# Optimization experiments

Measured on AMD Instinct MI355X. Metric: run time of the kernel, lower is better.

The kernel has to match this reference:

```python
import jax, jax.numpy as jnp
import numpy as np

N, D = 8192, 1024
Q = 4096
DK = 512
DV = 256


def setup_inputs() -> dict:
    key = jax.random.key(0)
    k1, k2, k3, k4, k5, k6 = jax.random.split(key, 6)
    return {
        "search_x": jax.random.normal(k1, (N, D), dtype=jnp.float32),
        "search_y": jax.random.normal(k2, (N, DV), dtype=jnp.float32),
        "query_x": jax.random.normal(k3, (Q, D), dtype=jnp.float32),
        "mask": jax.random.randint(k4, (Q, N), 0, 2, dtype=jnp.int64),
        "Wk": jax.random.normal(k5, (D, DK), dtype=jnp.float32) / np.sqrt(D),
        "Wq": jax.random.normal(k6, (D, DK), dtype=jnp.float32) / np.sqrt(D),
    }


def reference(search_x, search_y, query_x, mask, Wk, Wq):
    # key/query modules: bias-free linear projections (n_keys == 1 after _ensure_key_shape)
    keys = search_x @ Wk            # [N, DK]
    qk = query_x @ Wq               # [Q, DK]
    scale = 1.0 / jnp.sqrt(jnp.asarray(DK, dtype=keys.dtype))
    logits = (qk @ keys.T) * scale  # [Q, N]  (== broadcast mul+sum in original)
    # masked softmax over the search dimension (dim=1)
    m = mask > 0                    # [Q, N]
    neg = jnp.finfo(logits.dtype).min
    p = jax.nn.softmax(jnp.where(m, logits, neg), axis=1)
    p = jnp.where(m, p, 0.0)
    # values = noop_value_module(search_x, search_y) = search_y  [N, DV]
    res = p @ search_y              # [Q, DV]
    return res[:, None, :]          # [Q, n_keys=1, DV], matching original output shape
```

## Files before the change

### kernel.cpp

```cpp
#include <hip/hip_runtime.h>
#include <hip/hip_fp16.h>

typedef _Float16 half4v __attribute__((ext_vector_type(4)));
typedef _Float16 half8v __attribute__((ext_vector_type(8)));
typedef float floatx4 __attribute__((ext_vector_type(4)));

__global__ __launch_bounds__(256) void k_f32_to_f16(const float* __restrict__ in,
                                                    _Float16* __restrict__ out, int n) {
    int i = (blockIdx.x * 256 + threadIdx.x) * 4;
    if (i >= n) return;
    float4 v = *(const float4*)(in + i);
    half4v h;
    h[0] = (_Float16)v.x; h[1] = (_Float16)v.y; h[2] = (_Float16)v.z; h[3] = (_Float16)v.w;
    *(half4v*)(out + i) = h;
}

__global__ __launch_bounds__(256) void k_transpose_f16(const float* __restrict__ in,
                                                       _Float16* __restrict__ out,
                                                       int R, int C) {
    __shared__ float tile[32][33];
    int bc = blockIdx.x * 32;
    int br = blockIdx.y * 32;
    int tx = threadIdx.x & 31, ty = threadIdx.x >> 5;
#pragma unroll
    for (int i = 0; i < 32; i += 8)
        tile[ty + i][tx] = in[(size_t)(br + ty + i) * C + bc + tx];
    __syncthreads();
#pragma unroll
    for (int i = 0; i < 32; i += 8)
        out[(size_t)(bc + ty + i) * R + br + tx] = (_Float16)tile[tx][ty + i];
}

template <bool OUT_F16>
__global__ __launch_bounds__(256) void k_gemm_nt(const _Float16* __restrict__ A,
                                                 const _Float16* __restrict__ B,
                                                 void* __restrict__ C,
                                                 int M, int N, int K, int kChunk,
                                                 float scale) {
    __shared__ _Float16 As[128 * 72];
    __shared__ _Float16 Bs[128 * 72];
    const int tid  = threadIdx.x;
    const int lane = tid & 63;
    const int wave = tid >> 6;
    const int wm   = (wave >> 1) * 64;
    const int wn   = (wave & 1) * 64;
    const int quad = lane >> 4;
    const int lr   = lane & 15;
    const long m0 = (long)blockIdx.y * 128;
    const long n0 = (long)blockIdx.x * 128;
    const int kBegin = blockIdx.z * kChunk;
    const int kEnd   = kBegin + kChunk;

    floatx4 acc[4][4] = {};

    const int sr = tid >> 3;
    const int sc = (tid & 7) * 8;

    for (int kt = kBegin; kt < kEnd; kt += 64) {
        const _Float16* Ap = A + (m0 + sr) * (long)K + kt + sc;
        const _Float16* Bp = B + (n0 + sr) * (long)K + kt + sc;
        uint4 av[4], bv[4];
#pragma unroll
        for (int r = 0; r < 4; ++r) {
            av[r] = *(const uint4*)(Ap + (long)(r * 32) * K);
            bv[r] = *(const uint4*)(Bp + (long)(r * 32) * K);
        }
#pragma unroll
        for (int r = 0; r < 4; ++r) {
            *(uint4*)&As[(sr + r * 32) * 72 + sc] = av[r];
            *(uint4*)&Bs[(sr + r * 32) * 72 + sc] = bv[r];
        }
        __syncthreads();

#pragma unroll
        for (int kk = 0; kk < 64; kk += 32) {
            half8v af[4], bf[4];
#pragma unroll
            for (int i = 0; i < 4; ++i)
                af[i] = *(const half8v*)&As[(wm + i * 16 + lr) * 72 + kk + quad * 8];
#pragma unroll
            for (int j = 0; j < 4; ++j)
                bf[j] = *(const half8v*)&Bs[(wn + j * 16 + lr) * 72 + kk + quad * 8];
#pragma unroll
            for (int i = 0; i < 4; ++i)
#pragma unroll
                for (int j = 0; j < 4; ++j)
                    acc[i][j] = __builtin_amdgcn_mfma_f32_16x16x32_f16(af[i], bf[j], acc[i][j], 0, 0, 0);
        }
        __syncthreads();
    }

#pragma unroll
    for (int i = 0; i < 4; ++i) {
        long rbase = m0 + wm + i * 16 + quad * 4;
#pragma unroll
        for (int j = 0; j < 4; ++j) {
            long col = n0 + wn + j * 16 + lr;
#pragma unroll
            for (int r = 0; r < 4; ++r) {
                float val = acc[i][j][r] * scale;
                if (OUT_F16)
                    ((_Float16*)C)[(rbase + r) * (long)N + col] = (_Float16)val;
                else
                    atomicAdd((float*)C + (rbase + r) * (long)N + col, val);
            }
        }
    }
}

__global__ __launch_bounds__(256) void k_softmax(_Float16* __restrict__ logits,
                                                 const int* __restrict__ mask) {
    const int q   = blockIdx.x;
    const int tid = threadIdx.x;
    _Float16* row   = logits + (size_t)q * 8192;
    const int* mrow = mask + (size_t)q * 8192;

    float v[32];
    unsigned mb = 0;
    float lmax = -3.0e38f;
#pragma unroll
    for (int i = 0; i < 8; ++i) {
        int base = i * 1024 + tid * 4;
        int4 mm  = *(const int4*)(mrow + base);
        half4v h = *(const half4v*)(row + base);
#pragma unroll
        for (int j = 0; j < 4; ++j) v[i * 4 + j] = (float)h[j];
        if (mm.x > 0) { mb |= 1u << (i * 4 + 0); lmax = fmaxf(lmax, v[i * 4 + 0]); }
        if (mm.y > 0) { mb |= 1u << (i * 4 + 1); lmax = fmaxf(lmax, v[i * 4 + 1]); }
        if (mm.z > 0) { mb |= 1u << (i * 4 + 2); lmax = fmaxf(lmax, v[i * 4 + 2]); }
        if (mm.w > 0) { mb |= 1u << (i * 4 + 3); lmax = fmaxf(lmax, v[i * 4 + 3]); }
    }
#pragma unroll
    for (int off = 32; off > 0; off >>= 1) lmax = fmaxf(lmax, __shfl_xor(lmax, off, 64));
    __shared__ float redmax[4], redsum[4];
    if ((tid & 63) == 0) redmax[tid >> 6] = lmax;
    __syncthreads();
    lmax = fmaxf(fmaxf(redmax[0], redmax[1]), fmaxf(redmax[2], redmax[3]));

    float lsum = 0.f;
#pragma unroll
    for (int i = 0; i < 32; ++i) {
        float e = ((mb >> i) & 1u) ? __expf(v[i] - lmax) : 0.f;
        v[i] = e;
        lsum += e;
    }
#pragma unroll
    for (int off = 32; off > 0; off >>= 1) lsum += __shfl_xor(lsum, off, 64);
    if ((tid & 63) == 0) redsum[tid >> 6] = lsum;
    __syncthreads();
    lsum = redsum[0] + redsum[1] + redsum[2] + redsum[3];
    float inv = lsum > 0.f ? 1.f / lsum : 0.f;

#pragma unroll
    for (int i = 0; i < 8; ++i) {
        int base = i * 1024 + tid * 4;
        half4v h;
#pragma unroll
        for (int j = 0; j < 4; ++j) h[j] = (_Float16)(v[i * 4 + j] * inv);
        *(half4v*)(row + base) = h;
    }
}

extern "C" void kernel_launch(void* const* d_in, const int* in_sizes, int n_in,
                              void* d_out, int out_size, void* d_ws, size_t ws_size,
                              hipStream_t stream) {
    const float* search_x = (const float*)d_in[0];
    const float* search_y = (const float*)d_in[1];
    const float* query_x  = (const float*)d_in[2];
    const int*   mask     = (const int*)d_in[3];
    const float* Wk       = (const float*)d_in[4];
    const float* Wq       = (const float*)d_in[5];
    (void)in_sizes; (void)n_in; (void)ws_size;

    char* p = (char*)d_ws;
    _Float16* xh   = (_Float16*)p; p += (size_t)8192 * 1024 * 2;
    _Float16* qh   = (_Float16*)p; p += (size_t)4096 * 1024 * 2;
    _Float16* wkT  = (_Float16*)p; p += (size_t)512 * 1024 * 2;
    _Float16* wqT  = (_Float16*)p; p += (size_t)512 * 1024 * 2;
    _Float16* yT   = (_Float16*)p; p += (size_t)256 * 8192 * 2;
    _Float16* keys = (_Float16*)p; p += (size_t)8192 * 512 * 2;
    _Float16* qk   = (_Float16*)p; p += (size_t)4096 * 512 * 2;
    _Float16* lg   = (_Float16*)p; p += (size_t)4096 * 8192 * 2;

    k_f32_to_f16<<<8192, 256, 0, stream>>>(search_x, xh, 8192 * 1024);
    k_f32_to_f16<<<4096, 256, 0, stream>>>(query_x, qh, 4096 * 1024);
    k_transpose_f16<<<dim3(16, 32), 256, 0, stream>>>(Wk, wkT, 1024, 512);
    k_transpose_f16<<<dim3(16, 32), 256, 0, stream>>>(Wq, wqT, 1024, 512);
    k_transpose_f16<<<dim3(8, 256), 256, 0, stream>>>(search_y, yT, 8192, 256);

    k_gemm_nt<true><<<dim3(4, 64, 1), 256, 0, stream>>>(xh, wkT, keys, 8192, 512, 1024, 1024, 1.0f);
    k_gemm_nt<true><<<dim3(4, 32, 1), 256, 0, stream>>>(qh, wqT, qk, 4096, 512, 1024, 1024, 1.0f);
    k_gemm_nt<true><<<dim3(64, 32, 1), 256, 0, stream>>>(qk, keys, lg, 4096, 8192, 512, 512,
                                                         0.04419417382415922f);
    k_softmax<<<4096, 256, 0, stream>>>(lg, mask);
    hipMemsetAsync(d_out, 0, (size_t)out_size * sizeof(float), stream);
    k_gemm_nt<false><<<dim3(2, 32, 8), 256, 0, stream>>>(lg, yT, (float*)d_out, 4096, 256, 8192,
                                                         1024, 1.0f);
}
```

Baseline: 384.3 us.

## Use direct global-to-LDS async loads with XOR swizzle; replace atomics with split-K reduce

The GEMM tile loads now use global_load_lds to copy 16-byte chunks straight into shared memory. The LDS layout drops its padding in favour of an XOR swizzle so that MFMA fragment reads avoid bank conflicts. The final split-K GEMM writes per-slice partial sums to a workspace, and a separate reduction kernel adds the 8 partials, which removes the memset and the float atomics. This costs extra workspace traffic for the partials and one more launch, and it relies on the 16-byte LDS DMA path being supported.

```diff
diff --git a/kernel.cpp b/kernel.cpp
--- a/kernel.cpp
+++ b/kernel.cpp
@@ -4,6 +4,14 @@
 typedef _Float16 half4v __attribute__((ext_vector_type(4)));
 typedef _Float16 half8v __attribute__((ext_vector_type(8)));
 typedef float floatx4 __attribute__((ext_vector_type(4)));
+
+#define GLOBAL_AS __attribute__((address_space(1)))
+#define LDS_AS __attribute__((address_space(3)))
+
+__device__ __forceinline__ void async_copy16(const _Float16* g, _Float16* l) {
+    __builtin_amdgcn_global_load_lds((const GLOBAL_AS unsigned int*)g,
+                                     (LDS_AS unsigned int*)l, 16, 0, 0);
+}
 
 __global__ __launch_bounds__(256) void k_f32_to_f16(const float* __restrict__ in,
                                                     _Float16* __restrict__ out, int n) {
@@ -31,14 +39,14 @@
         out[(size_t)(bc + ty + i) * R + br + tx] = (_Float16)tile[tx][ty + i];
 }
 
-template <bool OUT_F16>
+template <int OUT_MODE>
 __global__ __launch_bounds__(256) void k_gemm_nt(const _Float16* __restrict__ A,
                                                  const _Float16* __restrict__ B,
                                                  void* __restrict__ C,
                                                  int M, int N, int K, int kChunk,
                                                  float scale) {
-    __shared__ _Float16 As[128 * 72];
-    __shared__ _Float16 Bs[128 * 72];
+    __shared__ __align__(16) _Float16 As[128 * 64];
+    __shared__ __align__(16) _Float16 Bs[128 * 64];
     const int tid  = threadIdx.x;
     const int lane = tid & 63;
     const int wave = tid >> 6;
@@ -53,34 +61,34 @@
 
     floatx4 acc[4][4] = {};
 
-    const int sr = tid >> 3;
-    const int sc = (tid & 7) * 8;
+    const int rl = lane >> 3;
+    const int gc = (lane & 7) ^ rl;
+    const long arow = m0 + wave * 32 + rl;
+    const long brow = n0 + wave * 32 + rl;
 
     for (int kt = kBegin; kt < kEnd; kt += 64) {
-        const _Float16* Ap = A + (m0 + sr) * (long)K + kt + sc;
-        const _Float16* Bp = B + (n0 + sr) * (long)K + kt + sc;
-        uint4 av[4], bv[4];
-#pragma unroll
-        for (int r = 0; r < 4; ++r) {
-            av[r] = *(const uint4*)(Ap + (long)(r * 32) * K);
-            bv[r] = *(const uint4*)(Bp + (long)(r * 32) * K);
-        }
-#pragma unroll
-        for (int r = 0; r < 4; ++r) {
-            *(uint4*)&As[(sr + r * 32) * 72 + sc] = av[r];
-            *(uint4*)&Bs[(sr + r * 32) * 72 + sc] = bv[r];
+        const _Float16* Ap = A + arow * (long)K + kt + gc * 8;
+        const _Float16* Bp = B + brow * (long)K + kt + gc * 8;
+        _Float16* Al = &As[(wave * 32) * 64];
+        _Float16* Bl = &Bs[(wave * 32) * 64];
+#pragma unroll
+        for (int i = 0; i < 4; ++i) {
+            async_copy16(Ap + (long)(i * 8) * K, Al + i * 8 * 64);
+            async_copy16(Bp + (long)(i * 8) * K, Bl + i * 8 * 64);
         }
         __syncthreads();
 
 #pragma unroll
         for (int kk = 0; kk < 64; kk += 32) {
             half8v af[4], bf[4];
+            const int cg = (kk >> 3) + quad;
+            const int sl = (cg ^ (lr & 7)) * 8;
 #pragma unroll
             for (int i = 0; i < 4; ++i)
-                af[i] = *(const half8v*)&As[(wm + i * 16 + lr) * 72 + kk + quad * 8];
+                af[i] = *(const half8v*)&As[(wm + i * 16 + lr) * 64 + sl];
 #pragma unroll
             for (int j = 0; j < 4; ++j)
-                bf[j] = *(const half8v*)&Bs[(wn + j * 16 + lr) * 72 + kk + quad * 8];
+                bf[j] = *(const half8v*)&Bs[(wn + j * 16 + lr) * 64 + sl];
 #pragma unroll
             for (int i = 0; i < 4; ++i)
 #pragma unroll
@@ -99,13 +107,26 @@
 #pragma unroll
             for (int r = 0; r < 4; ++r) {
                 float val = acc[i][j][r] * scale;
-                if (OUT_F16)
+                if (OUT_MODE == 0)
                     ((_Float16*)C)[(rbase + r) * (long)N + col] = (_Float16)val;
                 else
-                    atomicAdd((float*)C + (rbase + r) * (long)N + col, val);
+                    ((float*)C)[(size_t)blockIdx.z * M * N + (rbase + r) * (long)N + col] = val;
             }
         }
     }
+}
+
+__global__ __launch_bounds__(256) void k_reduce8(const float* __restrict__ part,
+                                                 float* __restrict__ out, int n) {
+    int i = (blockIdx.x * 256 + threadIdx.x) * 4;
+    if (i >= n) return;
+    float4 s = *(const float4*)(part + i);
+#pragma unroll
+    for (int z = 1; z < 8; ++z) {
+        float4 v = *(const float4*)(part + (size_t)z * n + i);
+        s.x += v.x; s.y += v.y; s.z += v.z; s.w += v.w;
+    }
+    *(float4*)(out + i) = s;
 }
 
 __global__ __launch_bounds__(256) void k_softmax(_Float16* __restrict__ logits,
@@ -170,7 +191,7 @@
     const int*   mask     = (const int*)d_in[3];
     const float* Wk       = (const float*)d_in[4];
     const float* Wq       = (const float*)d_in[5];
-    (void)in_sizes; (void)n_in; (void)ws_size;
+    (void)in_sizes; (void)n_in; (void)ws_size; (void)out_size;
 
     char* p = (char*)d_ws;
     _Float16* xh   = (_Float16*)p; p += (size_t)8192 * 1024 * 2;
@@ -181,6 +202,7 @@
     _Float16* keys = (_Float16*)p; p += (size_t)8192 * 512 * 2;
     _Float16* qk   = (_Float16*)p; p += (size_t)4096 * 512 * 2;
     _Float16* lg   = (_Float16*)p; p += (size_t)4096 * 8192 * 2;
+    float*    part = (float*)p;    p += (size_t)8 * 4096 * 256 * 4;
 
     k_f32_to_f16<<<8192, 256, 0, stream>>>(search_x, xh, 8192 * 1024);
     k_f32_to_f16<<<4096, 256, 0, stream>>>(query_x, qh, 4096 * 1024);
@@ -188,12 +210,11 @@
     k_transpose_f16<<<dim3(16, 32), 256, 0, stream>>>(Wq, wqT, 1024, 512);
     k_transpose_f16<<<dim3(8, 256), 256, 0, stream>>>(search_y, yT, 8192, 256);
 
-    k_gemm_nt<true><<<dim3(4, 64, 1), 256, 0, stream>>>(xh, wkT, keys, 8192, 512, 1024, 1024, 1.0f);
-    k_gemm_nt<true><<<dim3(4, 32, 1), 256, 0, stream>>>(qh, wqT, qk, 4096, 512, 1024, 1024, 1.0f);
-    k_gemm_nt<true><<<dim3(64, 32, 1), 256, 0, stream>>>(qk, keys, lg, 4096, 8192, 512, 512,
-                                                         0.04419417382415922f);
+    k_gemm_nt<0><<<dim3(4, 64, 1), 256, 0, stream>>>(xh, wkT, keys, 8192, 512, 1024, 1024, 1.0f);
+    k_gemm_nt<0><<<dim3(4, 32, 1), 256, 0, stream>>>(qh, wqT, qk, 4096, 512, 1024, 1024, 1.0f);
+    k_gemm_nt<0><<<dim3(64, 32, 1), 256, 0, stream>>>(qk, keys, lg, 4096, 8192, 512, 512,
+                                                      0.04419417382415922f);
     k_softmax<<<4096, 256, 0, stream>>>(lg, mask);
-    hipMemsetAsync(d_out, 0, (size_t)out_size * sizeof(float), stream);
-    k_gemm_nt<false><<<dim3(2, 32, 8), 256, 0, stream>>>(lg, yT, (float*)d_out, 4096, 256, 8192,
-                                                         1024, 1.0f);
-}
+    k_gemm_nt<1><<<dim3(2, 32, 8), 256, 0, stream>>>(lg, yT, part, 4096, 256, 8192, 1024, 1.0f);
+    k_reduce8<<<1024, 256, 0, stream>>>(part, (float*)d_out, 4096 * 256);
+}
```

Measured after the change: 367.1 us. -4.5%, faster.
